# Kernel optimization log

Measured on AMD Instinct MI355X. Metric: run time of the kernel, lower is better.

The kernel has to match this reference:

```python
import jax, jax.numpy as jnp
import numpy as np

B, N, H = 2, 2048, 1024
NUM_HEADS, HEAD_DIM = 16, 64
SCALE = HEAD_DIM ** -0.5


def setup_inputs() -> dict:
    key = jax.random.key(0)
    ks = jax.random.split(key, 9)
    hidden_states = jax.random.normal(ks[0], (B, N, H), dtype=jnp.float32)
    # ancestor-only mask: lower-triangular incl. diagonal (chain tree)
    tree_mask = jnp.tril(jnp.ones((N, N), dtype=jnp.int32))
    s = H ** -0.5
    Wq = jax.random.normal(ks[1], (H, NUM_HEADS * HEAD_DIM), dtype=jnp.float32) * s
    Wk = jax.random.normal(ks[2], (H, NUM_HEADS * HEAD_DIM), dtype=jnp.float32) * s
    Wv = jax.random.normal(ks[3], (H, NUM_HEADS * HEAD_DIM), dtype=jnp.float32) * s
    Wo = jax.random.normal(ks[4], (NUM_HEADS * HEAD_DIM, H), dtype=jnp.float32) * s
    bq = jnp.zeros((NUM_HEADS * HEAD_DIM,), dtype=jnp.float32)
    bk = jnp.zeros((NUM_HEADS * HEAD_DIM,), dtype=jnp.float32)
    bv = jnp.zeros((NUM_HEADS * HEAD_DIM,), dtype=jnp.float32)
    bo = jnp.zeros((H,), dtype=jnp.float32)
    return {"hidden_states": hidden_states, "tree_mask": tree_mask,
            "Wq": Wq, "bq": bq, "Wk": Wk, "bk": bk,
            "Wv": Wv, "bv": bv, "Wo": Wo, "bo": bo}


def reference(hidden_states, tree_mask, Wq, bq, Wk, bk, Wv, bv, Wo, bo):
    b, n, _ = hidden_states.shape
    q = (hidden_states @ Wq + bq).reshape(b, n, NUM_HEADS, HEAD_DIM)
    k = (hidden_states @ Wk + bk).reshape(b, n, NUM_HEADS, HEAD_DIM)
    v = (hidden_states @ Wv + bv).reshape(b, n, NUM_HEADS, HEAD_DIM)
    # scores: [b, heads, n, n]
    scores = jnp.einsum('bqhd,bkhd->bhqk', q, k) * SCALE
    neg_inf = jnp.finfo(scores.dtype).min
    scores = jnp.where(tree_mask[None, None, :, :] == 0, neg_inf, scores)
    attn = jax.nn.softmax(scores, axis=-1)  # dropout p=0.0 -> identity
    out = jnp.einsum('bhqk,bkhd->bqhd', attn, v).reshape(b, n, NUM_HEADS * HEAD_DIM)
    return out @ Wo + bo
```

## Files before the change

kernel.cpp:

```cpp
#include <hip/hip_runtime.h>
#include <hip/hip_bf16.h>
#include <stdint.h>

typedef unsigned short u16;
typedef short short8 __attribute__((ext_vector_type(8)));
typedef float f32x4 __attribute__((ext_vector_type(4)));
typedef u16 u16x4 __attribute__((ext_vector_type(4)));

#define SCLOG 0.18033688011112042f

static __device__ __forceinline__ u16 f2bf(float f) {
  unsigned u = __float_as_uint(f);
  unsigned rnd = 0x7fffu + ((u >> 16) & 1u);
  return (u16)((u + rnd) >> 16);
}

static __device__ __forceinline__ unsigned pk_bf16(float a, float b) {
  unsigned r;
  asm("v_cvt_pk_bf16_f32 %0, %1, %2" : "=v"(r) : "v"(a), "v"(b));
  return r;
}

static __device__ __forceinline__ void gload_lds16(const void* g, void* l) {
  __builtin_amdgcn_global_load_lds(
      (const __attribute__((address_space(1))) unsigned int*)g,
      (__attribute__((address_space(3))) unsigned int*)l, 16, 0, 0);
}

__global__ __launch_bounds__(256) void prep_kernel(
    const float* __restrict__ hs, const int* __restrict__ mask,
    const float* __restrict__ Wq, const float* __restrict__ Wk,
    const float* __restrict__ Wv, const float* __restrict__ Wo,
    u16* __restrict__ X, u16* __restrict__ WT,
    unsigned long long* __restrict__ bits) {
  __shared__ float tile[32][33];
  const int bid = blockIdx.x;
  const int tid = threadIdx.x;
  if (bid < 4096) {
    const int i = bid * 256 + tid;
    const float4 v = reinterpret_cast<const float4*>(hs)[i];
    u16x4 o;
    o[0] = f2bf(v.x); o[1] = f2bf(v.y); o[2] = f2bf(v.z); o[3] = f2bf(v.w);
    reinterpret_cast<u16x4*>(X)[i] = o;
  } else if (bid < 8192) {
    const int B = bid - 4096;
    const int z = B >> 10, y = (B >> 5) & 31, x = B & 31;
    const float* src = (z == 0) ? Wq : (z == 1) ? Wk : (z == 2) ? Wv : Wo;
    u16* dst = WT + (size_t)z * 1024 * 1024;
    const int row0 = y * 32, col0 = x * 32;
    const int tx = tid & 31, ty = tid >> 5;
#pragma unroll
    for (int i = 0; i < 4; ++i)
      tile[ty + i * 8][tx] = src[(size_t)(row0 + ty + i * 8) * 1024 + col0 + tx];
    __syncthreads();
#pragma unroll
    for (int i = 0; i < 4; ++i) {
      const int r = ty + i * 8;
      dst[(size_t)(col0 + r) * 1024 + row0 + tx] = f2bf(tile[tx][r]);
    }
  } else {
    const int gw = (bid - 8192) * 4 + (tid >> 6);
    const int lane = tid & 63;
    const int q = gw >> 5, w = gw & 31;
    const int mv = mask[(size_t)q * 2048 + w * 64 + lane];
    const unsigned long long bal = __ballot(mv != 0);
    if (lane == 0) bits[(size_t)q * 32 + w] = bal;
  }
}

__global__ __launch_bounds__(256) void gemm_qkv_kernel(
    const u16* __restrict__ X, const u16* __restrict__ WT,
    const float* __restrict__ bq, const float* __restrict__ bk, const float* __restrict__ bv,
    u16* __restrict__ Qb, u16* __restrict__ Kb, u16* __restrict__ Vb) {
  __shared__ u16 As[128 * 32];
  __shared__ u16 Bs[128 * 32];
  const int tid = threadIdx.x;
  const int lane = tid & 63, wid = tid >> 6;
  const int l15 = lane & 15, lg = lane >> 4;
  const int n0 = blockIdx.x * 128, m0 = blockIdx.y * 128;
  const int wr = wid >> 1, wc = wid & 1;

  f32x4 acc[4][4] = {};

  for (int kt = 0; kt < 32; ++kt) {
    __syncthreads();
#pragma unroll
    for (int p = 0; p < 2; ++p) {
      const int c = p * 256 + tid;
      const int r = c >> 2, ch = c & 3;
      gload_lds16(X + (size_t)(m0 + r) * 1024 + kt * 32 + ch * 8,
                  &As[(p * 256 + wid * 64) * 8]);
      gload_lds16(WT + (size_t)(n0 + r) * 1024 + kt * 32 + ch * 8,
                  &Bs[(p * 256 + wid * 64) * 8]);
    }
    __syncthreads();
    short8 af[4], bfr[4];
#pragma unroll
    for (int i = 0; i < 4; ++i) {
      af[i] = *reinterpret_cast<const short8*>(&As[(wr * 64 + i * 16 + l15) * 32 + lg * 8]);
      bfr[i] = *reinterpret_cast<const short8*>(&Bs[(wc * 64 + i * 16 + l15) * 32 + lg * 8]);
    }
#pragma unroll
    for (int i = 0; i < 4; ++i)
#pragma unroll
      for (int j = 0; j < 4; ++j)
        acc[i][j] = __builtin_amdgcn_mfma_f32_16x16x32_bf16(bfr[j], af[i], acc[i][j], 0, 0, 0);
  }

#pragma unroll
  for (int i = 0; i < 4; ++i) {
    const int m = m0 + wr * 64 + i * 16 + l15;
    const int bb = m >> 11, t = m & 2047;
#pragma unroll
    for (int j = 0; j < 4; ++j) {
      const int n = n0 + wc * 64 + j * 16 + lg * 4;
      const float* bsrc = (n < 1024) ? (bq + n) : (n < 2048) ? (bk + n - 1024) : (bv + n - 2048);
      const float4 b4 = *reinterpret_cast<const float4*>(bsrc);
      const float scl = (n < 1024) ? SCLOG : 1.0f;
      u16* dst = (n < 1024) ? Qb : (n < 2048) ? Kb : Vb;
      const int nl = n & 1023;
      const int hh = nl >> 6, d0 = nl & 63;
      uint2 pk;
      pk.x = pk_bf16((acc[i][j][0] + b4.x) * scl, (acc[i][j][1] + b4.y) * scl);
      pk.y = pk_bf16((acc[i][j][2] + b4.z) * scl, (acc[i][j][3] + b4.w) * scl);
      *reinterpret_cast<uint2*>(dst + ((size_t)(bb * 16 + hh) * 2048 + t) * 64 + d0) = pk;
    }
  }
}

__global__ __launch_bounds__(256) void transpose_v_kernel(const u16* __restrict__ Vb,
                                                          u16* __restrict__ VT) {
  __shared__ u16 tile[64][68];
  const int tid = threadIdx.x;
  const int tt = blockIdx.x & 31;
  const int bh = blockIdx.x >> 5;
  const size_t base = (size_t)bh * 2048 * 64;
  const int t0 = tt * 64;
#pragma unroll
  for (int p = 0; p < 2; ++p) {
    int i = p * 256 + tid;
    int row = i >> 3, ch = i & 7;
    *reinterpret_cast<short8*>(&tile[row][ch * 8]) =
        *reinterpret_cast<const short8*>(Vb + base + (size_t)(t0 + row) * 64 + ch * 8);
  }
  __syncthreads();
#pragma unroll
  for (int p = 0; p < 2; ++p) {
    int i = p * 256 + tid;
    int d = i >> 3, ch = i & 7;
    short8 v;
#pragma unroll
    for (int j = 0; j < 8; ++j) v[j] = tile[ch * 8 + j][d];
    *reinterpret_cast<short8*>(VT + base + (size_t)d * 2048 + t0 + ch * 8) = v;
  }
}

struct AttnState {
  f32x4 O[4];
  float l;
  short8 qf0, qf1;
};

static __device__ __forceinline__ void attn_tile(
    AttnState& st, const u16* __restrict__ Kb_, const u16* __restrict__ Vb_,
    u16* __restrict__ pwave, unsigned long long w,
    int l15, int lg, int slg) {
  f32x4 sT[4] = {};
  __builtin_amdgcn_s_setprio(1);
#pragma unroll
  for (int dc = 0; dc < 2; ++dc) {
    const short8 qv = dc ? st.qf1 : st.qf0;
#pragma unroll
    for (int sub = 0; sub < 4; ++sub) {
      const short8 kf = *reinterpret_cast<const short8*>(
          &Kb_[dc * 2048 + (sub * 16 + l15) * 32 + slg]);
      sT[sub] = __builtin_amdgcn_mfma_f32_16x16x32_bf16(kf, qv, sT[sub], 0, 0, 0);
    }
  }
  __builtin_amdgcn_s_setprio(0);

  if (!__all(w == ~0ull)) {
    const unsigned mlo = (unsigned)w, mhi = (unsigned)(w >> 32);
#pragma unroll
    for (int sub = 0; sub < 4; ++sub) {
      const unsigned f = ((sub & 2) ? mhi : mlo) >> ((sub & 1) * 16 + lg * 4);
#pragma unroll
      for (int r = 0; r < 4; ++r)
        sT[sub][r] = ((f >> r) & 1u) ? sT[sub][r] : -1e30f;
    }
  }

  float lsum = 0.f;
#pragma unroll
  for (int kc = 0; kc < 2; ++kc) {
#pragma unroll
    for (int s2 = 0; s2 < 2; ++s2) {
      const int sub = kc * 2 + s2;
      const float e0 = exp2f(sT[sub][0]);
      const float e1 = exp2f(sT[sub][1]);
      const float e2 = exp2f(sT[sub][2]);
      const float e3 = exp2f(sT[sub][3]);
      lsum += (e0 + e1) + (e2 + e3);
      uint2 pk;
      pk.x = pk_bf16(e0, e1);
      pk.y = pk_bf16(e2, e3);
      *reinterpret_cast<uint2*>(&pwave[l15 * 40 + s2 * 16 + lg * 4]) = pk;
    }
    const short8 pf = *reinterpret_cast<const short8*>(&pwave[l15 * 40 + lg * 8]);
    __builtin_amdgcn_s_setprio(1);
#pragma unroll
    for (int dt = 0; dt < 4; ++dt) {
      const short8 vf = *reinterpret_cast<const short8*>(
          &Vb_[kc * 2048 + (dt * 16 + l15) * 32 + slg]);
      st.O[dt] = __builtin_amdgcn_mfma_f32_16x16x32_bf16(vf, pf, st.O[dt], 0, 0, 0);
    }
    __builtin_amdgcn_s_setprio(0);
  }
  st.l += lsum;
}

__global__ __launch_bounds__(256, 4) void attn_kernel(
    const u16* __restrict__ Q, const u16* __restrict__ K, const u16* __restrict__ VT,
    const unsigned long long* __restrict__ MB, u16* __restrict__ AO) {
  __shared__ u16 K_lds[2][4096];
  __shared__ u16 V_lds[2][4096];
  __shared__ u16 p_lds[4][16][40];
  __shared__ unsigned actA_s, actB_s;

  const int tid = threadIdx.x;
  const int wid = tid >> 6, lane = tid & 63;
  const int l15 = lane & 15, lg = lane >> 4;

  const int wgid = blockIdx.x;
  const int x = wgid & 7, s = wgid >> 3;
  const int g = x + 8 * (s >> 5);
  const int qp = s & 31;
  const int h = g & 15, b = g >> 4;
  const int qA_t = qp, qB_t = 63 - qp;
  const size_t bh_off = ((size_t)(b * 16 + h)) * 2048 * 64;

  if (tid == 0) { actA_s = 0; actB_s = 0; }
  __syncthreads();
  {
    const int ktc = tid & 31, rg = tid >> 5;
    unsigned long long orA = 0, orB = 0;
#pragma unroll
    for (int i = 0; i < 4; ++i) {
      orA |= MB[(size_t)(qA_t * 32 + rg * 4 + i) * 32 + ktc];
      orB |= MB[(size_t)(qB_t * 32 + rg * 4 + i) * 32 + ktc];
    }
    if (orA) atomicOr(&actA_s, 1u << ktc);
    if (orB) atomicOr(&actB_s, 1u << ktc);
  }

  const int sid = wid >> 1;
  const int qt = sid ? qB_t : qA_t;
  const int q = qt * 32 + (wid & 1) * 16 + l15;

  AttnState st;
  {
    const short8* qp_ = reinterpret_cast<const short8*>(Q + bh_off + (size_t)q * 64);
    st.qf0 = qp_[lg]; st.qf1 = qp_[4 + lg];
#pragma unroll
    for (int dt = 0; dt < 4; ++dt) st.O[dt] = f32x4{};
    st.l = 0.f;
  }

  const int slg = (lg ^ ((l15 >> 1) & 3)) * 8;

  int offK[2], offV[2], ldsi[2];
#pragma unroll
  for (int p = 0; p < 2; ++p) {
    const int i = wid * 128 + p * 64 + lane;
    const int pc = i >> 8, row = (i >> 2) & 63, lgc = i & 3;
    const int lgs = lgc ^ ((i >> 3) & 3);
    offK[p] = row * 64 + pc * 32 + lgs * 8;
    offV[p] = row * 2048 + pc * 32 + lgs * 8;
    ldsi[p] = (wid * 128 + p * 64) * 8;
  }
  const u16* Kg = K + bh_off;
  const u16* Vg = VT + bh_off;
  u16* pwave = &p_lds[wid][0][0];

  __syncthreads();
  const unsigned actA = actA_s, actB = actB_s;
  const unsigned actW = sid ? actB : actA;
  unsigned rem = actA | actB;
  int buf = 0;

#define STAGE_TILE(bb, ktv)                                        \
  do {                                                             \
    const u16* ksrc_ = Kg + (ktv) * 64 * 64;                       \
    const u16* vsrc_ = Vg + (ktv) * 64;                            \
    _Pragma("unroll") for (int p_ = 0; p_ < 2; ++p_) {             \
      gload_lds16(ksrc_ + offK[p_], &K_lds[bb][ldsi[p_]]);         \
      gload_lds16(vsrc_ + offV[p_], &V_lds[bb][ldsi[p_]]);         \
    }                                                              \
  } while (0)

  if (rem) {
    int kt = __ffs(rem) - 1;
    unsigned long long w_cur = MB[(size_t)q * 32 + kt];
    STAGE_TILE(0, kt);
    __syncthreads();

    while (true) {
      rem &= rem - 1;
      int ktn = -1;
      unsigned long long w_next = 0;
      if (rem) {
        ktn = __ffs(rem) - 1;
        w_next = MB[(size_t)q * 32 + ktn];
        STAGE_TILE(buf ^ 1, ktn);
      }

      if ((actW >> kt) & 1u)
        attn_tile(st, &K_lds[buf][0], &V_lds[buf][0], pwave, w_cur, l15, lg, slg);

      if (ktn < 0) break;
      __syncthreads();
      buf ^= 1;
      kt = ktn;
      w_cur = w_next;
    }
  }
#undef STAGE_TILE

  {
    float lr = st.l;
    lr += __shfl_xor(lr, 16);
    lr += __shfl_xor(lr, 32);
    const float inv = (lr > 0.f) ? (1.0f / lr) : 0.f;
    u16* dst = AO + ((size_t)(b * 2048 + q)) * 1024 + h * 64;
#pragma unroll
    for (int dt = 0; dt < 4; ++dt) {
      uint2 pk;
      pk.x = pk_bf16(st.O[dt][0] * inv, st.O[dt][1] * inv);
      pk.y = pk_bf16(st.O[dt][2] * inv, st.O[dt][3] * inv);
      *reinterpret_cast<uint2*>(dst + dt * 16 + lg * 4) = pk;
    }
  }
}

__global__ __launch_bounds__(256) void gemm_out_kernel(
    const u16* __restrict__ A, const u16* __restrict__ BT,
    const float* __restrict__ bo, float* __restrict__ out) {
  __shared__ u16 As[128 * 32];
  __shared__ u16 Bs[128 * 32];
  const int tid = threadIdx.x;
  const int lane = tid & 63, wid = tid >> 6;
  const int l15 = lane & 15, lg = lane >> 4;
  const int n0 = blockIdx.x * 128, m0 = blockIdx.y * 128;
  const int wr = wid >> 1, wc = wid & 1;

  f32x4 acc[4][4] = {};

  for (int kt = 0; kt < 32; ++kt) {
    __syncthreads();
#pragma unroll
    for (int p = 0; p < 2; ++p) {
      const int c = p * 256 + tid;
      const int r = c >> 2, ch = c & 3;
      gload_lds16(A + (size_t)(m0 + r) * 1024 + kt * 32 + ch * 8,
                  &As[(p * 256 + wid * 64) * 8]);
      gload_lds16(BT + (size_t)(n0 + r) * 1024 + kt * 32 + ch * 8,
                  &Bs[(p * 256 + wid * 64) * 8]);
    }
    __syncthreads();
    short8 af[4], bfr[4];
#pragma unroll
    for (int i = 0; i < 4; ++i) {
      af[i] = *reinterpret_cast<const short8*>(&As[(wr * 64 + i * 16 + l15) * 32 + lg * 8]);
      bfr[i] = *reinterpret_cast<const short8*>(&Bs[(wc * 64 + i * 16 + l15) * 32 + lg * 8]);
    }
#pragma unroll
    for (int i = 0; i < 4; ++i)
#pragma unroll
      for (int j = 0; j < 4; ++j)
        acc[i][j] = __builtin_amdgcn_mfma_f32_16x16x32_bf16(bfr[j], af[i], acc[i][j], 0, 0, 0);
  }

#pragma unroll
  for (int i = 0; i < 4; ++i) {
    const int m = m0 + wr * 64 + i * 16 + l15;
#pragma unroll
    for (int j = 0; j < 4; ++j) {
      const int n = n0 + wc * 64 + j * 16 + lg * 4;
      const float4 b4 = *reinterpret_cast<const float4*>(bo + n);
      float4 o4;
      o4.x = acc[i][j][0] + b4.x;
      o4.y = acc[i][j][1] + b4.y;
      o4.z = acc[i][j][2] + b4.z;
      o4.w = acc[i][j][3] + b4.w;
      *reinterpret_cast<float4*>(out + (size_t)m * 1024 + n) = o4;
    }
  }
}

extern "C" void kernel_launch(void* const* d_in, const int* in_sizes, int n_in,
                              void* d_out, int out_size, void* d_ws, size_t ws_size,
                              hipStream_t stream) {
  (void)in_sizes; (void)n_in; (void)out_size; (void)ws_size;
  const float* hs = (const float*)d_in[0];
  const int* mask = (const int*)d_in[1];
  const float* Wq = (const float*)d_in[2];
  const float* bq = (const float*)d_in[3];
  const float* Wk = (const float*)d_in[4];
  const float* bk = (const float*)d_in[5];
  const float* Wv = (const float*)d_in[6];
  const float* bv = (const float*)d_in[7];
  const float* Wo = (const float*)d_in[8];
  const float* bo = (const float*)d_in[9];
  float* out = (float*)d_out;

  uint8_t* ws = (uint8_t*)d_ws;
  u16* X  = (u16*)(ws);
  u16* WT = (u16*)(ws + ((size_t)8 << 20));
  u16* Qb = (u16*)(ws + ((size_t)16 << 20));
  u16* Kb = (u16*)(ws + ((size_t)24 << 20));
  u16* Vb = (u16*)(ws + ((size_t)32 << 20));
  u16* AO = (u16*)(ws + ((size_t)40 << 20));
  unsigned long long* MB = (unsigned long long*)(ws + ((size_t)48 << 20));
  u16* VbT = X;

  prep_kernel<<<dim3(24576), dim3(256), 0, stream>>>(hs, mask, Wq, Wk, Wv, Wo, X, WT, MB);
  gemm_qkv_kernel<<<dim3(24, 32), dim3(256), 0, stream>>>(X, WT, bq, bk, bv, Qb, Kb, Vb);
  transpose_v_kernel<<<dim3(1024), dim3(256), 0, stream>>>(Vb, VbT);
  attn_kernel<<<dim3(1024), dim3(256), 0, stream>>>(Qb, Kb, VbT, MB, AO);
  gemm_out_kernel<<<dim3(8, 32), dim3(256), 0, stream>>>(AO, WT + (size_t)3072 * 1024, bo, out);
}
```

Measured before the change: 136.4 us.

## Process two 16-row query blocks per wave to reuse K/V LDS fragments

The attention workgroup shrinks from 4 waves to 2, and each wave now handles 32 query rows (two 16-row MFMA blocks) instead of 16. Every K and V fragment read from LDS feeds two MFMAs, which halves LDS reads per unit of work and gives the scheduler more independent MFMA chains. Each wave also issues twice as many global-to-LDS loads per tile. The cost is higher register pressure from the doubled accumulators, fewer waves per workgroup, and the launch bound moving to (128,2), which may reduce occupancy and latency hiding.

```diff
diff --git a/kernel.cpp b/kernel.cpp
--- a/kernel.cpp
+++ b/kernel.cpp
@@ -155,76 +155,101 @@
   }
 }
 
-struct AttnState {
-  f32x4 O[4];
-  float l;
-  short8 qf0, qf1;
-};
-
-static __device__ __forceinline__ void attn_tile(
-    AttnState& st, const u16* __restrict__ Kb_, const u16* __restrict__ Vb_,
-    u16* __restrict__ pwave, unsigned long long w,
+static __device__ __forceinline__ void attn_tile2(
+    f32x4 O0[4], f32x4 O1[4], float& l0, float& l1,
+    short8 q00, short8 q01, short8 q10, short8 q11,
+    const u16* __restrict__ Kb_, const u16* __restrict__ Vb_,
+    u16* __restrict__ pw0, u16* __restrict__ pw1,
+    unsigned long long w0, unsigned long long w1,
     int l15, int lg, int slg) {
-  f32x4 sT[4] = {};
+  f32x4 s0[4] = {}, s1[4] = {};
   __builtin_amdgcn_s_setprio(1);
 #pragma unroll
   for (int dc = 0; dc < 2; ++dc) {
-    const short8 qv = dc ? st.qf1 : st.qf0;
+    const short8 qa = dc ? q01 : q00;
+    const short8 qb = dc ? q11 : q10;
 #pragma unroll
     for (int sub = 0; sub < 4; ++sub) {
       const short8 kf = *reinterpret_cast<const short8*>(
           &Kb_[dc * 2048 + (sub * 16 + l15) * 32 + slg]);
-      sT[sub] = __builtin_amdgcn_mfma_f32_16x16x32_bf16(kf, qv, sT[sub], 0, 0, 0);
+      s0[sub] = __builtin_amdgcn_mfma_f32_16x16x32_bf16(kf, qa, s0[sub], 0, 0, 0);
+      s1[sub] = __builtin_amdgcn_mfma_f32_16x16x32_bf16(kf, qb, s1[sub], 0, 0, 0);
     }
   }
   __builtin_amdgcn_s_setprio(0);
 
-  if (!__all(w == ~0ull)) {
-    const unsigned mlo = (unsigned)w, mhi = (unsigned)(w >> 32);
+  if (!__all(w0 == ~0ull)) {
+    const unsigned mlo = (unsigned)w0, mhi = (unsigned)(w0 >> 32);
 #pragma unroll
     for (int sub = 0; sub < 4; ++sub) {
       const unsigned f = ((sub & 2) ? mhi : mlo) >> ((sub & 1) * 16 + lg * 4);
 #pragma unroll
       for (int r = 0; r < 4; ++r)
-        sT[sub][r] = ((f >> r) & 1u) ? sT[sub][r] : -1e30f;
-    }
-  }
-
-  float lsum = 0.f;
+        s0[sub][r] = ((f >> r) & 1u) ? s0[sub][r] : -1e30f;
+    }
+  }
+  if (!__all(w1 == ~0ull)) {
+    const unsigned mlo = (unsigned)w1, mhi = (unsigned)(w1 >> 32);
+#pragma unroll
+    for (int sub = 0; sub < 4; ++sub) {
+      const unsigned f = ((sub & 2) ? mhi : mlo) >> ((sub & 1) * 16 + lg * 4);
+#pragma unroll
+      for (int r = 0; r < 4; ++r)
+        s1[sub][r] = ((f >> r) & 1u) ? s1[sub][r] : -1e30f;
+    }
+  }
+
+  float ls0 = 0.f, ls1 = 0.f;
 #pragma unroll
   for (int kc = 0; kc < 2; ++kc) {
 #pragma unroll
     for (int s2 = 0; s2 < 2; ++s2) {
       const int sub = kc * 2 + s2;
-      const float e0 = exp2f(sT[sub][0]);
-      const float e1 = exp2f(sT[sub][1]);
-      const float e2 = exp2f(sT[sub][2]);
-      const float e3 = exp2f(sT[sub][3]);
-      lsum += (e0 + e1) + (e2 + e3);
-      uint2 pk;
-      pk.x = pk_bf16(e0, e1);
-      pk.y = pk_bf16(e2, e3);
-      *reinterpret_cast<uint2*>(&pwave[l15 * 40 + s2 * 16 + lg * 4]) = pk;
-    }
-    const short8 pf = *reinterpret_cast<const short8*>(&pwave[l15 * 40 + lg * 8]);
+      {
+        const float e0 = exp2f(s0[sub][0]);
+        const float e1 = exp2f(s0[sub][1]);
+        const float e2 = exp2f(s0[sub][2]);
+        const float e3 = exp2f(s0[sub][3]);
+        ls0 += (e0 + e1) + (e2 + e3);
+        uint2 pk;
+        pk.x = pk_bf16(e0, e1);
+        pk.y = pk_bf16(e2, e3);
+        *reinterpret_cast<uint2*>(&pw0[l15 * 40 + s2 * 16 + lg * 4]) = pk;
+      }
+      {
+        const float e0 = exp2f(s1[sub][0]);
+        const float e1 = exp2f(s1[sub][1]);
+        const float e2 = exp2f(s1[sub][2]);
+        const float e3 = exp2f(s1[sub][3]);
+        ls1 += (e0 + e1) + (e2 + e3);
+        uint2 pk;
+        pk.x = pk_bf16(e0, e1);
+        pk.y = pk_bf16(e2, e3);
+        *reinterpret_cast<uint2*>(&pw1[l15 * 40 + s2 * 16 + lg * 4]) = pk;
+      }
+    }
+    const short8 pf0 = *reinterpret_cast<const short8*>(&pw0[l15 * 40 + lg * 8]);
+    const short8 pf1 = *reinterpret_cast<const short8*>(&pw1[l15 * 40 + lg * 8]);
     __builtin_amdgcn_s_setprio(1);
 #pragma unroll
     for (int dt = 0; dt < 4; ++dt) {
       const short8 vf = *reinterpret_cast<const short8*>(
           &Vb_[kc * 2048 + (dt * 16 + l15) * 32 + slg]);
-      st.O[dt] = __builtin_amdgcn_mfma_f32_16x16x32_bf16(vf, pf, st.O[dt], 0, 0, 0);
+      O0[dt] = __builtin_amdgcn_mfma_f32_16x16x32_bf16(vf, pf0, O0[dt], 0, 0, 0);
+      O1[dt] = __builtin_amdgcn_mfma_f32_16x16x32_bf16(vf, pf1, O1[dt], 0, 0, 0);
     }
     __builtin_amdgcn_s_setprio(0);
   }
-  st.l += lsum;
-}
-
-__global__ __launch_bounds__(256, 4) void attn_kernel(
+  l0 += ls0;
+  l1 += ls1;
+}
+
+__global__ __launch_bounds__(128, 2) void attn_kernel(
     const u16* __restrict__ Q, const u16* __restrict__ K, const u16* __restrict__ VT,
     const unsigned long long* __restrict__ MB, u16* __restrict__ AO) {
   __shared__ u16 K_lds[2][4096];
   __shared__ u16 V_lds[2][4096];
-  __shared__ u16 p_lds[4][16][40];
+  __shared__ u16 p_lds[2][2][16][40];
   __shared__ unsigned actA_s, actB_s;
 
   const int tid = threadIdx.x;
@@ -245,46 +270,48 @@
     const int ktc = tid & 31, rg = tid >> 5;
     unsigned long long orA = 0, orB = 0;
 #pragma unroll
-    for (int i = 0; i < 4; ++i) {
-      orA |= MB[(size_t)(qA_t * 32 + rg * 4 + i) * 32 + ktc];
-      orB |= MB[(size_t)(qB_t * 32 + rg * 4 + i) * 32 + ktc];
+    for (int i = 0; i < 8; ++i) {
+      orA |= MB[(size_t)(qA_t * 32 + rg * 8 + i) * 32 + ktc];
+      orB |= MB[(size_t)(qB_t * 32 + rg * 8 + i) * 32 + ktc];
     }
     if (orA) atomicOr(&actA_s, 1u << ktc);
     if (orB) atomicOr(&actB_s, 1u << ktc);
   }
 
-  const int sid = wid >> 1;
-  const int qt = sid ? qB_t : qA_t;
-  const int q = qt * 32 + (wid & 1) * 16 + l15;
-
-  AttnState st;
+  const int qt = wid ? qB_t : qA_t;
+  const int q0 = qt * 32 + l15;
+  const int q1 = qt * 32 + 16 + l15;
+
+  f32x4 O0[4] = {}, O1[4] = {};
+  float l0 = 0.f, l1 = 0.f;
+  short8 q00, q01, q10, q11;
   {
-    const short8* qp_ = reinterpret_cast<const short8*>(Q + bh_off + (size_t)q * 64);
-    st.qf0 = qp_[lg]; st.qf1 = qp_[4 + lg];
-#pragma unroll
-    for (int dt = 0; dt < 4; ++dt) st.O[dt] = f32x4{};
-    st.l = 0.f;
+    const short8* qpa = reinterpret_cast<const short8*>(Q + bh_off + (size_t)q0 * 64);
+    const short8* qpb = reinterpret_cast<const short8*>(Q + bh_off + (size_t)q1 * 64);
+    q00 = qpa[lg]; q01 = qpa[4 + lg];
+    q10 = qpb[lg]; q11 = qpb[4 + lg];
   }
 
   const int slg = (lg ^ ((l15 >> 1) & 3)) * 8;
 
-  int offK[2], offV[2], ldsi[2];
-#pragma unroll
-  for (int p = 0; p < 2; ++p) {
-    const int i = wid * 128 + p * 64 + lane;
+  int offK[4], offV[4], ldsi[4];
+#pragma unroll
+  for (int p = 0; p < 4; ++p) {
+    const int i = wid * 256 + p * 64 + lane;
     const int pc = i >> 8, row = (i >> 2) & 63, lgc = i & 3;
     const int lgs = lgc ^ ((i >> 3) & 3);
     offK[p] = row * 64 + pc * 32 + lgs * 8;
     offV[p] = row * 2048 + pc * 32 + lgs * 8;
-    ldsi[p] = (wid * 128 + p * 64) * 8;
+    ldsi[p] = (wid * 256 + p * 64) * 8;
   }
   const u16* Kg = K + bh_off;
   const u16* Vg = VT + bh_off;
-  u16* pwave = &p_lds[wid][0][0];
+  u16* pw0 = &p_lds[wid][0][0][0];
+  u16* pw1 = &p_lds[wid][1][0][0];
 
   __syncthreads();
   const unsigned actA = actA_s, actB = actB_s;
-  const unsigned actW = sid ? actB : actA;
+  const unsigned actW = wid ? actB : actA;
   unsigned rem = actA | actB;
   int buf = 0;
 
@@ -292,7 +319,7 @@
   do {                                                             \
     const u16* ksrc_ = Kg + (ktv) * 64 * 64;                       \
     const u16* vsrc_ = Vg + (ktv) * 64;                            \
-    _Pragma("unroll") for (int p_ = 0; p_ < 2; ++p_) {             \
+    _Pragma("unroll") for (int p_ = 0; p_ < 4; ++p_) {             \
       gload_lds16(ksrc_ + offK[p_], &K_lds[bb][ldsi[p_]]);         \
       gload_lds16(vsrc_ + offV[p_], &V_lds[bb][ldsi[p_]]);         \
     }                                                              \
@@ -300,43 +327,62 @@
 
   if (rem) {
     int kt = __ffs(rem) - 1;
-    unsigned long long w_cur = MB[(size_t)q * 32 + kt];
+    unsigned long long w0_cur = MB[(size_t)q0 * 32 + kt];
+    unsigned long long w1_cur = MB[(size_t)q1 * 32 + kt];
     STAGE_TILE(0, kt);
     __syncthreads();
 
     while (true) {
       rem &= rem - 1;
       int ktn = -1;
-      unsigned long long w_next = 0;
+      unsigned long long w0_next = 0, w1_next = 0;
       if (rem) {
         ktn = __ffs(rem) - 1;
-        w_next = MB[(size_t)q * 32 + ktn];
+        w0_next = MB[(size_t)q0 * 32 + ktn];
+        w1_next = MB[(size_t)q1 * 32 + ktn];
         STAGE_TILE(buf ^ 1, ktn);
       }
 
       if ((actW >> kt) & 1u)
-        attn_tile(st, &K_lds[buf][0], &V_lds[buf][0], pwave, w_cur, l15, lg, slg);
+        attn_tile2(O0, O1, l0, l1, q00, q01, q10, q11,
+                   &K_lds[buf][0], &V_lds[buf][0], pw0, pw1,
+                   w0_cur, w1_cur, l15, lg, slg);
 
       if (ktn < 0) break;
       __syncthreads();
       buf ^= 1;
       kt = ktn;
-      w_cur = w_next;
+      w0_cur = w0_next;
+      w1_cur = w1_next;
     }
   }
 #undef STAGE_TILE
 
   {
-    float lr = st.l;
+    float lr = l0;
     lr += __shfl_xor(lr, 16);
     lr += __shfl_xor(lr, 32);
     const float inv = (lr > 0.f) ? (1.0f / lr) : 0.f;
-    u16* dst = AO + ((size_t)(b * 2048 + q)) * 1024 + h * 64;
+    u16* dst = AO + ((size_t)(b * 2048 + q0)) * 1024 + h * 64;
 #pragma unroll
     for (int dt = 0; dt < 4; ++dt) {
       uint2 pk;
-      pk.x = pk_bf16(st.O[dt][0] * inv, st.O[dt][1] * inv);
-      pk.y = pk_bf16(st.O[dt][2] * inv, st.O[dt][3] * inv);
+      pk.x = pk_bf16(O0[dt][0] * inv, O0[dt][1] * inv);
+      pk.y = pk_bf16(O0[dt][2] * inv, O0[dt][3] * inv);
+      *reinterpret_cast<uint2*>(dst + dt * 16 + lg * 4) = pk;
+    }
+  }
+  {
+    float lr = l1;
+    lr += __shfl_xor(lr, 16);
+    lr += __shfl_xor(lr, 32);
+    const float inv = (lr > 0.f) ? (1.0f / lr) : 0.f;
+    u16* dst = AO + ((size_t)(b * 2048 + q1)) * 1024 + h * 64;
+#pragma unroll
+    for (int dt = 0; dt < 4; ++dt) {
+      uint2 pk;
+      pk.x = pk_bf16(O1[dt][0] * inv, O1[dt][1] * inv);
+      pk.y = pk_bf16(O1[dt][2] * inv, O1[dt][3] * inv);
       *reinterpret_cast<uint2*>(dst + dt * 16 + lg * 4) = pk;
     }
   }
@@ -426,6 +472,6 @@
   prep_kernel<<<dim3(24576), dim3(256), 0, stream>>>(hs, mask, Wq, Wk, Wv, Wo, X, WT, MB);
   gemm_qkv_kernel<<<dim3(24, 32), dim3(256), 0, stream>>>(X, WT, bq, bk, bv, Qb, Kb, Vb);
   transpose_v_kernel<<<dim3(1024), dim3(256), 0, stream>>>(Vb, VbT);
-  attn_kernel<<<dim3(1024), dim3(256), 0, stream>>>(Qb, Kb, VbT, MB, AO);
+  attn_kernel<<<dim3(1024), dim3(128), 0, stream>>>(Qb, Kb, VbT, MB, AO);
   gemm_out_kernel<<<dim3(8, 32), dim3(256), 0, stream>>>(AO, WT + (size_t)3072 * 1024, bo, out);
 }
```

New measurement: 144.9 us. 1.06x slower.
